# Kernel tuning notes

Hardware: AMD Instinct MI355X
Metric: run time of the kernel (lower is better)

Reference implementation:

```python
import jax, jax.numpy as jnp
from jax import lax
import numpy as np

N_GROUP = 1024   # number of FPS centroids
N_SAMPLE = 32    # neighbors per ball query
RADIUS = 0.2
BN_EPS = 1e-5    # torch BatchNorm2d default, training-mode batch stats
MLP = [64, 64, 128]
IN_CH = 6        # 3 relative xyz + 3 point features


def setup_inputs() -> dict:
    key = jax.random.key(0)
    ks = jax.random.split(key, 8)
    B, N = 16, 4096
    out = {
        "xyz": jax.random.uniform(ks[0], (B, N, 3), dtype=jnp.float32),
        "point_feature": jax.random.normal(ks[1], (B, N, 3), dtype=jnp.float32),
    }
    last = IN_CH
    for li, oc in enumerate(MLP):
        out[f"w{li}"] = jax.random.normal(ks[2 + li], (oc, last), dtype=jnp.float32) / np.float32(np.sqrt(last))
        out[f"b{li}"] = jnp.zeros((oc,), jnp.float32)
        out[f"g{li}"] = jnp.ones((oc,), jnp.float32)
        out[f"be{li}"] = jnp.zeros((oc,), jnp.float32)
        last = oc
    return out


def _fps(xyz, n_group):
    # Farthest point sampling. xyz: [B, N, 3] -> idx [B, n_group]
    B, N, _ = xyz.shape

    def step(carry, _):
        dist, farthest = carry                      # [B,N], [B]
        centroid = jnp.take_along_axis(xyz, farthest[:, None, None], axis=1)  # [B,1,3]
        d = jnp.sum((xyz - centroid) ** 2, -1)      # [B,N]
        dist = jnp.minimum(dist, d)
        nxt = jnp.argmax(dist, -1).astype(jnp.int32)
        return (dist, nxt), farthest

    init = (jnp.full((B, N), 1e10, xyz.dtype), jnp.zeros((B,), jnp.int32))
    _, idxs = lax.scan(step, init, None, length=n_group)
    return idxs.T                                    # [B, n_group]


def _ball_query(xyz, new_xyz, radius, n_sample):
    # xyz: [B,N,3], new_xyz: [B,S,3] -> idx [B,S,n_sample]
    B, N, _ = xyz.shape
    sqr = jnp.sum((new_xyz[:, :, None, :] - xyz[:, None, :, :]) ** 2, -1)  # [B,S,N]
    idx = jnp.where(sqr > radius * radius, N, jnp.arange(N, dtype=jnp.int32))
    idx = jnp.sort(idx, axis=-1)[:, :, :n_sample]    # closest-index fill like torch impl
    first = idx[:, :, :1]
    return jnp.where(idx == N, first, idx)


def reference(xyz, point_feature, w0, b0, g0, be0, w1, b1, g1, be1, w2, b2, g2, be2):
    B = xyz.shape[0]
    fps_idx = _fps(xyz, N_GROUP)                     # [B,S]
    bi = jnp.arange(B)[:, None]
    new_xyz = xyz[bi, fps_idx]                       # [B,S,3]

    idx = _ball_query(xyz, new_xyz, RADIUS, N_SAMPLE)  # [B,S,K]
    bii = jnp.arange(B)[:, None, None]
    grouped_xyz = xyz[bii, idx] - new_xyz[:, :, None, :]   # [B,S,K,3] centered
    grouped_feat = point_feature[bii, idx]                 # [B,S,K,3]
    x = jnp.concatenate([grouped_xyz, grouped_feat], -1)   # [B,S,K,6]

    # 1x1 Conv2d == per-point linear; BN over all dims but channel (training stats)
    for w, b, g, be in ((w0, b0, g0, be0), (w1, b1, g1, be1), (w2, b2, g2, be2)):
        x = jnp.einsum('bskc,oc->bsko', x, w) + b
        mu = x.mean((0, 1, 2))
        var = x.var((0, 1, 2))
        x = g * (x - mu) * lax.rsqrt(var + BN_EPS) + be
        x = jax.nn.relu(x)

    new_feature = x.max(axis=2)                      # max over n_sample -> [B,S,128]
    return new_xyz, new_feature
```

## Files before the change

kernel.cpp:

```cpp
#include <hip/hip_runtime.h>

constexpr int BATCH = 16;
constexpr int NPT   = 4096;
constexpr int NGRP  = 1024;
constexpr int NSMP  = 32;
constexpr int NPTS  = BATCH * NGRP * NSMP;
constexpr int PBLK  = 4096;
constexpr int NG    = BATCH * NGRP;

__device__ __forceinline__ float sqd(float dx, float dy, float dz) {
  return __fadd_rn(__fadd_rn(__fmul_rn(dx, dx), __fmul_rn(dy, dy)), __fmul_rn(dz, dz));
}

template <int CTRL, int RM>
__device__ __forceinline__ unsigned long long dpp_lvl(unsigned long long P) {
  const int lo = (int)(unsigned int)P;
  const int hi = (int)(unsigned int)(P >> 32);
  const int tlo = __builtin_amdgcn_update_dpp(lo, lo, CTRL, RM, 0xF, false);
  const int thi = __builtin_amdgcn_update_dpp(hi, hi, CTRL, RM, 0xF, false);
  const unsigned long long T =
      ((unsigned long long)(unsigned int)thi << 32) | (unsigned int)tlo;
  return (T > P) ? T : P;
}

__global__ __launch_bounds__(256) void fps_kernel(const float* __restrict__ xyz,
                                                  float* __restrict__ out) {
  __shared__ float sx[NPT], sy[NPT], sz[NPT];
  __shared__ float cq[NGRP * 3];
  __shared__ unsigned int ex[2][5][4];
  const int b = blockIdx.x;
  const int t = threadIdx.x;
  const float* src = xyz + (size_t)b * NPT * 3;
  for (int i = t; i < NPT; i += 256) {
    sx[i] = src[i * 3 + 0];
    sy[i] = src[i * 3 + 1];
    sz[i] = src[i * 3 + 2];
  }
  __syncthreads();
  float px[16], py[16], pz[16], dist[16];
  #pragma unroll
  for (int j = 0; j < 16; ++j) {
    const int p = j * 256 + t;
    px[j] = sx[p]; py[j] = sy[p]; pz[j] = sz[p];
    dist[j] = 1e10f;
  }
  const int w = t >> 6;
  float cx = sx[0], cy = sy[0], cz = sz[0];
  for (int step = 0; step < NGRP; ++step) {
    if (t == 0) {
      cq[step * 3 + 0] = cx;
      cq[step * 3 + 1] = cy;
      cq[step * 3 + 2] = cz;
    }
    float bestd = -1.0f; int bi = 0x7fffffff;
    #pragma unroll
    for (int j = 0; j < 16; ++j) {
      float d = sqd(px[j] - cx, py[j] - cy, pz[j] - cz);
      d = fminf(dist[j], d);
      dist[j] = d;
      if (d > bestd) { bestd = d; bi = j * 256 + t; }
    }
    const int myidx = bi;
    const unsigned long long myP =
        ((unsigned long long)__float_as_uint(bestd) << 32) |
        (unsigned long long)(unsigned int)~myidx;
    const float mx = sx[myidx], my_ = sy[myidx], mz = sz[myidx];
    unsigned long long P = myP;
    P = dpp_lvl<0xB1, 0xF>(P);
    P = dpp_lvl<0x4E, 0xF>(P);
    P = dpp_lvl<0x141, 0xF>(P);
    P = dpp_lvl<0x140, 0xF>(P);
    P = dpp_lvl<0x142, 0xA>(P);
    P = dpp_lvl<0x143, 0xC>(P);
    const unsigned int flo = (unsigned int)__builtin_amdgcn_readlane((int)(unsigned int)P, 63);
    const unsigned int fhi =
        (unsigned int)__builtin_amdgcn_readlane((int)(unsigned int)(P >> 32), 63);
    const unsigned long long PF = ((unsigned long long)fhi << 32) | flo;
    const int pb = step & 1;
    if (myP == PF) {
      ex[pb][0][w] = fhi;
      ex[pb][1][w] = flo;
      ex[pb][2][w] = __float_as_uint(mx);
      ex[pb][3][w] = __float_as_uint(my_);
      ex[pb][4][w] = __float_as_uint(mz);
    }
    __syncthreads();
    const unsigned int* e = &ex[pb][0][0];
    unsigned long long best = ((unsigned long long)e[0] << 32) | e[4];
    cx = __uint_as_float(e[8]);
    cy = __uint_as_float(e[12]);
    cz = __uint_as_float(e[16]);
    #pragma unroll
    for (int k = 1; k < 4; ++k) {
      const unsigned long long pk_ = ((unsigned long long)e[k] << 32) | e[4 + k];
      if (pk_ > best) {
        best = pk_;
        cx = __uint_as_float(e[8 + k]);
        cy = __uint_as_float(e[12 + k]);
        cz = __uint_as_float(e[16 + k]);
      }
    }
  }
  __syncthreads();
  float* outx = out + (size_t)b * NGRP * 3;
  for (int i = t; i < NGRP * 3; i += 256) outx[i] = cq[i];
}

__global__ __launch_bounds__(256) void ballq_kernel(const float* __restrict__ xyz,
                                                    const float* __restrict__ out,
                                                    int* __restrict__ idxg) {
  __shared__ float sx[NPT], sy[NPT], sz[NPT];
  const int b = blockIdx.x >> 4;
  const int sub = blockIdx.x & 15;
  const float* src = xyz + (size_t)b * NPT * 3;
  for (int i = threadIdx.x; i < NPT; i += 256) {
    sx[i] = src[i * 3 + 0];
    sy[i] = src[i * 3 + 1];
    sz[i] = src[i * 3 + 2];
  }
  __syncthreads();
  const int lane = threadIdx.x & 63;
  const int w = threadIdx.x >> 6;
  const float R2 = __fmul_rn(0.2f, 0.2f);
  for (int gi = 0; gi < 16; ++gi) {
    const int s = sub * 64 + w * 16 + gi;
    const float* c = out + ((size_t)b * NGRP + s) * 3;
    const float nx = c[0], ny = c[1], nz = c[2];
    int* og = idxg + ((size_t)b * NGRP + s) * NSMP;
    int cnt = 0, firstP = -1;
    for (int base = 0; base < NPT; base += 64) {
      const int p = base + lane;
      const float dsq = sqd(nx - sx[p], ny - sy[p], nz - sz[p]);
      const bool inr = (dsq <= R2);
      unsigned long long m = __ballot(inr);
      if (firstP < 0 && m) firstP = base + (int)__builtin_ctzll(m);
      const int rank = (int)__popcll(m & ((1ull << lane) - 1ull));
      if (inr) {
        const int pos = cnt + rank;
        if (pos < NSMP) og[pos] = p;
      }
      cnt += (int)__popcll(m);
      if (cnt >= NSMP) break;
    }
    if (cnt < NSMP) {
      for (int pos = cnt + lane; pos < NSMP; pos += 64) og[pos] = firstP;
    }
  }
}

__global__ void transpose_w3(const float* __restrict__ w3, float* __restrict__ w3t) {
  const int i = blockIdx.x * 256 + threadIdx.x;
  if (i < 128 * 64) {
    const int o = i >> 6, c = i & 63;
    w3t[c * 128 + o] = w3[i];
  }
}

__device__ __forceinline__ void gather6(const float* __restrict__ xyz, const float* __restrict__ pf,
                                        const float* __restrict__ nxyz, const int* __restrict__ idxg,
                                        int tid, float in[6]) {
  const int g = tid >> 5;
  const int b = g >> 10;
  const int i = idxg[tid];
  const float* P = xyz + ((size_t)b * NPT + i) * 3;
  const float* C = nxyz + (size_t)g * 3;
  in[0] = P[0] - C[0];
  in[1] = P[1] - C[1];
  in[2] = P[2] - C[2];
  const float* F = pf + ((size_t)b * NPT + i) * 3;
  in[3] = F[0]; in[4] = F[1]; in[5] = F[2];
}

__device__ __forceinline__ void layer1h(const float in[6], const float* __restrict__ w1,
                                        const float* __restrict__ b1, const float* __restrict__ ss1,
                                        float h1[64]) {
  #pragma unroll
  for (int o = 0; o < 64; ++o) {
    float a = b1[o];
    #pragma unroll
    for (int cc = 0; cc < 6; ++cc) a = fmaf(in[cc], w1[o * 6 + cc], a);
    h1[o] = fmaxf(0.0f, fmaf(a, ss1[o], ss1[64 + o]));
  }
}

__device__ __forceinline__ void zb_stats64(const float* zb, float* __restrict__ part,
                                           int chbase, int nch, int t, int blk) {
  const int c = t >> 1, h = t & 1;
  const float* row = zb + c * 129 + h * 64;
  float s = 0.0f, q = 0.0f;
  for (int i = 0; i < 64; ++i) {
    const float v = row[i];
    s += v;
    q = fmaf(v, v, q);
  }
  s += __shfl_xor(s, 1);
  q += __shfl_xor(q, 1);
  if (h == 0) {
    part[(size_t)(chbase + c) * PBLK + blk]       = s;
    part[(size_t)(nch + chbase + c) * PBLK + blk] = q;
  }
}

__device__ __forceinline__ void zb_stats_mm(const float* zb, float* __restrict__ part,
                                            float* __restrict__ pmax, float* __restrict__ pmin,
                                            int chbase, int nch, int t, int blk) {
  const int c = t >> 1, h = t & 1;
  const float* row = zb + c * 129 + h * 64;
  float s = 0.0f, q = 0.0f;
  float mx0 = -3.4e38f, mn0 = 3.4e38f, mx1 = -3.4e38f, mn1 = 3.4e38f;
  for (int i = 0; i < 32; ++i) {
    const float v = row[i];
    s += v; q = fmaf(v, v, q);
    mx0 = fmaxf(mx0, v); mn0 = fminf(mn0, v);
  }
  for (int i = 32; i < 64; ++i) {
    const float v = row[i];
    s += v; q = fmaf(v, v, q);
    mx1 = fmaxf(mx1, v); mn1 = fminf(mn1, v);
  }
  s += __shfl_xor(s, 1);
  q += __shfl_xor(q, 1);
  if (h == 0) {
    part[(size_t)(chbase + c) * PBLK + blk]       = s;
    part[(size_t)(nch + chbase + c) * PBLK + blk] = q;
  }
  const size_t g0 = (size_t)blk * 4 + 2 * h;
  pmax[g0 * 128 + chbase + c]       = mx0;
  pmax[(g0 + 1) * 128 + chbase + c] = mx1;
  pmin[g0 * 128 + chbase + c]       = mn0;
  pmin[(g0 + 1) * 128 + chbase + c] = mn1;
}

__global__ __launch_bounds__(256) void mom1_kernel(const float* __restrict__ xyz,
                                                   const float* __restrict__ pf,
                                                   const float* __restrict__ nxyz,
                                                   const int* __restrict__ idxg,
                                                   float* __restrict__ part) {
  const int t = threadIdx.x;
  const int base = blockIdx.x * 512 + t;
  float acc[27];
  #pragma unroll
  for (int k = 0; k < 27; ++k) acc[k] = 0.0f;
  #pragma unroll
  for (int pp = 0; pp < 2; ++pp) {
    float in[6];
    gather6(xyz, pf, nxyz, idxg, base + pp * 256, in);
    #pragma unroll
    for (int i = 0; i < 6; ++i) acc[i] += in[i];
    int k = 6;
    #pragma unroll
    for (int i = 0; i < 6; ++i)
      #pragma unroll
      for (int j = i; j < 6; ++j) { acc[k] = fmaf(in[i], in[j], acc[k]); ++k; }
  }
  #pragma unroll
  for (int off = 1; off < 64; off <<= 1) {
    #pragma unroll
    for (int k = 0; k < 27; ++k) acc[k] += __shfl_xor(acc[k], off);
  }
  const int lane = t & 63, w = t >> 6;
  if (lane == 0) {
    const int slot = blockIdx.x * 4 + w;
    #pragma unroll
    for (int k = 0; k < 27; ++k) part[k * 4096 + slot] = acc[k];
  }
}

__global__ __launch_bounds__(256) void momred_kernel(const float* __restrict__ part,
                                                     double* __restrict__ dsum) {
  const int c = blockIdx.x;
  const int t = threadIdx.x;
  double s = 0.0;
  for (int i = t; i < 4096; i += 256) s += (double)part[c * 4096 + i];
  #pragma unroll
  for (int off = 1; off < 64; off <<= 1) s += __shfl_xor(s, off);
  __shared__ double ls[4];
  const int lane = t & 63, w = t >> 6;
  if (lane == 0) ls[w] = s;
  __syncthreads();
  if (t == 0) dsum[c] = ls[0] + ls[1] + ls[2] + ls[3];
}

__global__ __launch_bounds__(64) void finalize1_kernel(const double* __restrict__ dsum,
                                                       const float* __restrict__ w1,
                                                       const float* __restrict__ b1,
                                                       const float* __restrict__ g,
                                                       const float* __restrict__ be,
                                                       float* __restrict__ ss) {
  __shared__ double sm[27];
  const int t = threadIdx.x;
  if (t < 27) sm[t] = dsum[t];
  __syncthreads();
  const double N = (double)NPTS;
  double wv[6];
  #pragma unroll
  for (int i = 0; i < 6; ++i) wv[i] = (double)w1[t * 6 + i];
  double mean_wx = 0.0;
  #pragma unroll
  for (int i = 0; i < 6; ++i) mean_wx += wv[i] * sm[i];
  mean_wx /= N;
  const double bb = (double)b1[t];
  const double mu = mean_wx + bb;
  double qq = 0.0;
  int k = 6;
  #pragma unroll
  for (int i = 0; i < 6; ++i)
    #pragma unroll
    for (int j = i; j < 6; ++j) {
      qq += (i == j ? 1.0 : 2.0) * wv[i] * wv[j] * (sm[k] / N);
      ++k;
    }
  const double Ez2 = qq + 2.0 * bb * mean_wx + bb * bb;
  const double var = Ez2 - mu * mu;
  const double inv = 1.0 / sqrt(var + 1e-5);
  ss[t]      = (float)((double)g[t] * inv);
  ss[64 + t] = (float)((double)be[t] - (double)g[t] * mu * inv);
}

__global__ __launch_bounds__(256) void reduce_kernel(const float* __restrict__ part, int nblk, int nch,
                                                     const float* __restrict__ g, const float* __restrict__ be,
                                                     float* __restrict__ ss) {
  const int c = blockIdx.x;
  const int t = threadIdx.x;
  double s = 0.0, q = 0.0;
  for (int i = t; i < nblk; i += 256) {
    s += (double)part[(size_t)c * nblk + i];
    q += (double)part[(size_t)(nch + c) * nblk + i];
  }
  #pragma unroll
  for (int off = 1; off < 64; off <<= 1) {
    s += __shfl_xor(s, off);
    q += __shfl_xor(q, off);
  }
  __shared__ double ls[4], lq[4];
  const int lane = t & 63, w = t >> 6;
  if (lane == 0) { ls[w] = s; lq[w] = q; }
  __syncthreads();
  if (t == 0) {
    const double S = ls[0] + ls[1] + ls[2] + ls[3];
    const double Q = lq[0] + lq[1] + lq[2] + lq[3];
    const double n = (double)NPTS;
    const double mu = S / n;
    const double var = Q / n - mu * mu;
    const double inv = 1.0 / sqrt(var + 1e-5);
    ss[c]       = (float)((double)g[c] * inv);
    ss[nch + c] = (float)((double)be[c] - (double)g[c] * mu * inv);
  }
}

__global__ __launch_bounds__(128) void pass2_kernel(const float* __restrict__ xyz, const float* __restrict__ pf,
                                                    const float* __restrict__ nxyz, const int* __restrict__ idxg,
                                                    const float* __restrict__ w1, const float* __restrict__ b1,
                                                    const float* __restrict__ ss1,
                                                    const float* __restrict__ w2, const float* __restrict__ b2,
                                                    float* __restrict__ part) {
  __shared__ float zb[64 * 129];
  const int t = threadIdx.x;
  const int tid = blockIdx.x * 128 + t;
  float in[6];
  gather6(xyz, pf, nxyz, idxg, tid, in);
  float h1[64];
  layer1h(in, w1, b1, ss1, h1);
  for (int o = 0; o < 64; ++o) {
    float a = b2[o];
    #pragma unroll
    for (int cc = 0; cc < 64; ++cc) a = fmaf(h1[cc], w2[o * 64 + cc], a);
    zb[o * 129 + t] = a;
  }
  __syncthreads();
  zb_stats64(zb, part, 0, 64, t, blockIdx.x);
}

__device__ __forceinline__ void compute_z3(const float* __restrict__ xyz, const float* __restrict__ pf,
                                           const float* __restrict__ nxyz, const int* __restrict__ idxg,
                                           const float* __restrict__ w1, const float* __restrict__ b1,
                                           const float* __restrict__ ss1,
                                           const float* __restrict__ w2, const float* __restrict__ b2,
                                           const float* __restrict__ ss2,
                                           const float* __restrict__ w3t, const float* __restrict__ b3,
                                           float* shm, int t, int tid, float acc[128]) {
  float in[6];
  gather6(xyz, pf, nxyz, idxg, tid, in);
  float h1[64];
  layer1h(in, w1, b1, ss1, h1);
  float* hrow = shm + t * 65;
  for (int o = 0; o < 64; ++o) {
    float a = b2[o];
    #pragma unroll
    for (int cc = 0; cc < 64; ++cc) a = fmaf(h1[cc], w2[o * 64 + cc], a);
    hrow[o] = fmaxf(0.0f, fmaf(a, ss2[o], ss2[64 + o]));
  }
  #pragma unroll
  for (int o = 0; o < 128; ++o) acc[o] = b3[o];
  for (int cc = 0; cc < 64; ++cc) {
    const float hc = hrow[cc];
    const float* wrow = w3t + cc * 128;
    #pragma unroll
    for (int o = 0; o < 128; ++o) acc[o] = fmaf(hc, wrow[o], acc[o]);
  }
}

__global__ __launch_bounds__(128) void pass3_kernel(const float* __restrict__ xyz, const float* __restrict__ pf,
                                                    const float* __restrict__ nxyz, const int* __restrict__ idxg,
                                                    const float* __restrict__ w1, const float* __restrict__ b1,
                                                    const float* __restrict__ ss1,
                                                    const float* __restrict__ w2, const float* __restrict__ b2,
                                                    const float* __restrict__ ss2,
                                                    const float* __restrict__ w3t, const float* __restrict__ b3,
                                                    float* __restrict__ part,
                                                    float* __restrict__ pmax, float* __restrict__ pmin) {
  __shared__ float shm[8320];
  const int t = threadIdx.x;
  const int tid = blockIdx.x * 128 + t;
  float acc[128];
  compute_z3(xyz, pf, nxyz, idxg, w1, b1, ss1, w2, b2, ss2, w3t, b3, shm, t, tid, acc);
  __syncthreads();
  #pragma unroll
  for (int o = 0; o < 64; ++o) shm[o * 129 + t] = acc[o];
  __syncthreads();
  if (pmax) zb_stats_mm(shm, part, pmax, pmin, 0, 128, t, blockIdx.x);
  else      zb_stats64(shm, part, 0, 128, t, blockIdx.x);
  __syncthreads();
  #pragma unroll
  for (int o = 0; o < 64; ++o) shm[o * 129 + t] = acc[64 + o];
  __syncthreads();
  if (pmax) zb_stats_mm(shm, part, pmax, pmin, 64, 128, t, blockIdx.x);
  else      zb_stats64(shm, part, 64, 128, t, blockIdx.x);
}

__global__ __launch_bounds__(256) void pass4f_kernel(const float* __restrict__ pmax,
                                                     const float* __restrict__ pmin,
                                                     const float* __restrict__ ss3,
                                                     float* __restrict__ outF) {
  const int i = blockIdx.x * 256 + threadIdx.x;
  const int c = i & 127;
  const float a = ss3[c], bb = ss3[128 + c];
  const float z = (a >= 0.0f) ? pmax[i] : pmin[i];
  outF[i] = fmaxf(0.0f, fmaf(z, a, bb));
}

__global__ __launch_bounds__(128) void pass4_kernel(const float* __restrict__ xyz, const float* __restrict__ pf,
                                                    const float* __restrict__ nxyz, const int* __restrict__ idxg,
                                                    const float* __restrict__ w1, const float* __restrict__ b1,
                                                    const float* __restrict__ ss1,
                                                    const float* __restrict__ w2, const float* __restrict__ b2,
                                                    const float* __restrict__ ss2,
                                                    const float* __restrict__ w3t, const float* __restrict__ b3,
                                                    const float* __restrict__ ss3,
                                                    float* __restrict__ outF) {
  __shared__ float shm[8320];
  const int t = threadIdx.x;
  const int tid = blockIdx.x * 128 + t;
  float acc[128];
  compute_z3(xyz, pf, nxyz, idxg, w1, b1, ss1, w2, b2, ss2, w3t, b3, shm, t, tid, acc);
  #pragma unroll
  for (int o = 0; o < 128; ++o)
    acc[o] = fmaxf(0.0f, fmaf(acc[o], ss3[o], ss3[128 + o]));
  __syncthreads();
  const int c4 = t & 63, gp = t >> 6;
  #pragma unroll
  for (int o = 0; o < 64; ++o) shm[o * 129 + t] = acc[o];
  __syncthreads();
  #pragma unroll
  for (int gs = 0; gs < 2; ++gs) {
    const int g = gp * 2 + gs;
    const float* row = shm + c4 * 129 + g * 32;
    float m = row[0];
    for (int i = 1; i < 32; ++i) m = fmaxf(m, row[i]);
    outF[((size_t)blockIdx.x * 4 + g) * 128 + c4] = m;
  }
  __syncthreads();
  #pragma unroll
  for (int o = 0; o < 64; ++o) shm[o * 129 + t] = acc[64 + o];
  __syncthreads();
  #pragma unroll
  for (int gs = 0; gs < 2; ++gs) {
    const int g = gp * 2 + gs;
    const float* row = shm + c4 * 129 + g * 32;
    float m = row[0];
    for (int i = 1; i < 32; ++i) m = fmaxf(m, row[i]);
    outF[((size_t)blockIdx.x * 4 + g) * 128 + 64 + c4] = m;
  }
}

extern "C" void kernel_launch(void* const* d_in, const int* in_sizes, int n_in,
                              void* d_out, int out_size, void* d_ws, size_t ws_size,
                              hipStream_t stream) {
  (void)in_sizes; (void)n_in; (void)out_size;
  const float* xyz = (const float*)d_in[0];
  const float* pf  = (const float*)d_in[1];
  const float* w1  = (const float*)d_in[2];
  const float* b1  = (const float*)d_in[3];
  const float* g1  = (const float*)d_in[4];
  const float* be1 = (const float*)d_in[5];
  const float* w2  = (const float*)d_in[6];
  const float* b2  = (const float*)d_in[7];
  const float* g2  = (const float*)d_in[8];
  const float* be2 = (const float*)d_in[9];
  const float* w3  = (const float*)d_in[10];
  const float* b3  = (const float*)d_in[11];
  const float* g3  = (const float*)d_in[12];
  const float* be3 = (const float*)d_in[13];
  float* out = (float*)d_out;

  int*    idxg = (int*)d_ws;
  float*  p1   = (float*)((char*)d_ws + (size_t)NPTS * 4);
  float*  ss1  = p1 + (size_t)PBLK * 128;
  float*  p2   = ss1 + 128;
  float*  ss2  = p2 + (size_t)PBLK * 128;
  float*  p3   = ss2 + 128;
  float*  ss3  = p3 + (size_t)PBLK * 256;
  float*  w3t  = ss3 + 256;
  double* dsum = (double*)(w3t + 8192);
  float*  pmax = (float*)(dsum + 32);
  float*  pmin = pmax + (size_t)NG * 128;
  const size_t needed = (size_t)((char*)(pmin + (size_t)NG * 128) - (char*)d_ws);
  const bool fast4 = (ws_size >= needed);

  transpose_w3<<<32, 256, 0, stream>>>(w3, w3t);
  fps_kernel<<<BATCH, 256, 0, stream>>>(xyz, out);
  ballq_kernel<<<BATCH * 16, 256, 0, stream>>>(xyz, out, idxg);
  mom1_kernel<<<1024, 256, 0, stream>>>(xyz, pf, out, idxg, p1);
  momred_kernel<<<27, 256, 0, stream>>>(p1, dsum);
  finalize1_kernel<<<1, 64, 0, stream>>>(dsum, w1, b1, g1, be1, ss1);
  pass2_kernel<<<PBLK, 128, 0, stream>>>(xyz, pf, out, idxg, w1, b1, ss1, w2, b2, p2);
  reduce_kernel<<<64, 256, 0, stream>>>(p2, PBLK, 64, g2, be2, ss2);
  pass3_kernel<<<PBLK, 128, 0, stream>>>(xyz, pf, out, idxg, w1, b1, ss1, w2, b2, ss2, w3t, b3, p3,
                                         fast4 ? pmax : nullptr, fast4 ? pmin : nullptr);
  reduce_kernel<<<128, 256, 0, stream>>>(p3, PBLK, 128, g3, be3, ss3);
  float* outF = out + (size_t)BATCH * NGRP * 3;
  if (fast4) {
    pass4f_kernel<<<(NG * 128) / 256, 256, 0, stream>>>(pmax, pmin, ss3, outF);
  } else {
    pass4_kernel<<<PBLK, 128, 0, stream>>>(xyz, pf, out, idxg, w1, b1, ss1, w2, b2, ss2, w3t, b3, ss3,
                                           outF);
  }
}
```

Measured before the change: 1.383 ms.

## Fuse layer-1 moment stats into ball query and cache layer-2 preactivations in bf16

Computes the first-layer input moment sums inside the ball-query kernel from shared-memory coordinates, which removes the separate mom1 kernel and its global gather. Pass2 now also stores the layer-2 pre-activations as bf16 in workspace, and pass3 reads them back instead of recomputing the gather plus layers 1-2. That trades a 64x64 matmul per point for a bandwidth-bound bf16 read and write, and lowers the precision of the stored intermediate, which can shift results slightly.

```diff
diff --git a/kernel.cpp b/kernel.cpp
--- a/kernel.cpp
+++ b/kernel.cpp
@@ -1,4 +1,5 @@
 #include <hip/hip_runtime.h>
+#include <hip/hip_bf16.h>
 
 constexpr int BATCH = 16;
 constexpr int NPT   = 4096;
@@ -107,9 +108,13 @@
 }
 
 __global__ __launch_bounds__(256) void ballq_kernel(const float* __restrict__ xyz,
+                                                    const float* __restrict__ pf,
                                                     const float* __restrict__ out,
-                                                    int* __restrict__ idxg) {
+                                                    int* __restrict__ idxg,
+                                                    float* __restrict__ part) {
   __shared__ float sx[NPT], sy[NPT], sz[NPT];
+  __shared__ int   sel[64 * NSMP];
+  __shared__ float cent[64][3];
   const int b = blockIdx.x >> 4;
   const int sub = blockIdx.x & 15;
   const float* src = xyz + (size_t)b * NPT * 3;
@@ -123,10 +128,13 @@
   const int w = threadIdx.x >> 6;
   const float R2 = __fmul_rn(0.2f, 0.2f);
   for (int gi = 0; gi < 16; ++gi) {
-    const int s = sub * 64 + w * 16 + gi;
+    const int g = w * 16 + gi;
+    const int s = sub * 64 + g;
     const float* c = out + ((size_t)b * NGRP + s) * 3;
     const float nx = c[0], ny = c[1], nz = c[2];
+    if (lane == 0) { cent[g][0] = nx; cent[g][1] = ny; cent[g][2] = nz; }
     int* og = idxg + ((size_t)b * NGRP + s) * NSMP;
+    int* sg = sel + g * NSMP;
     int cnt = 0, firstP = -1;
     for (int base = 0; base < NPT; base += 64) {
       const int p = base + lane;
@@ -137,14 +145,50 @@
       const int rank = (int)__popcll(m & ((1ull << lane) - 1ull));
       if (inr) {
         const int pos = cnt + rank;
-        if (pos < NSMP) og[pos] = p;
+        if (pos < NSMP) { og[pos] = p; sg[pos] = p; }
       }
       cnt += (int)__popcll(m);
       if (cnt >= NSMP) break;
     }
     if (cnt < NSMP) {
-      for (int pos = cnt + lane; pos < NSMP; pos += 64) og[pos] = firstP;
-    }
+      for (int pos = cnt + lane; pos < NSMP; pos += 64) { og[pos] = firstP; sg[pos] = firstP; }
+    }
+  }
+  __syncthreads();
+  float acc[27];
+  #pragma unroll
+  for (int k = 0; k < 27; ++k) acc[k] = 0.0f;
+  const float* pfb = pf + (size_t)b * NPT * 3;
+  const int g2 = threadIdx.x >> 2;
+  const float c0 = cent[g2][0], c1 = cent[g2][1], c2 = cent[g2][2];
+  #pragma unroll
+  for (int ii = 0; ii < 8; ++ii) {
+    const int si = threadIdx.x * 8 + ii;
+    const int i = sel[si];
+    float in[6];
+    in[0] = sx[i] - c0;
+    in[1] = sy[i] - c1;
+    in[2] = sz[i] - c2;
+    in[3] = pfb[i * 3 + 0];
+    in[4] = pfb[i * 3 + 1];
+    in[5] = pfb[i * 3 + 2];
+    #pragma unroll
+    for (int k = 0; k < 6; ++k) acc[k] += in[k];
+    int k = 6;
+    #pragma unroll
+    for (int a = 0; a < 6; ++a)
+      #pragma unroll
+      for (int bb = a; bb < 6; ++bb) { acc[k] = fmaf(in[a], in[bb], acc[k]); ++k; }
+  }
+  #pragma unroll
+  for (int off = 1; off < 64; off <<= 1) {
+    #pragma unroll
+    for (int k = 0; k < 27; ++k) acc[k] += __shfl_xor(acc[k], off);
+  }
+  if (lane == 0) {
+    const int slot = blockIdx.x * 4 + w;
+    #pragma unroll
+    for (int k = 0; k < 27; ++k) part[k * 1024 + slot] = acc[k];
   }
 }
 
@@ -231,47 +275,12 @@
   pmin[(g0 + 1) * 128 + chbase + c] = mn1;
 }
 
-__global__ __launch_bounds__(256) void mom1_kernel(const float* __restrict__ xyz,
-                                                   const float* __restrict__ pf,
-                                                   const float* __restrict__ nxyz,
-                                                   const int* __restrict__ idxg,
-                                                   float* __restrict__ part) {
-  const int t = threadIdx.x;
-  const int base = blockIdx.x * 512 + t;
-  float acc[27];
-  #pragma unroll
-  for (int k = 0; k < 27; ++k) acc[k] = 0.0f;
-  #pragma unroll
-  for (int pp = 0; pp < 2; ++pp) {
-    float in[6];
-    gather6(xyz, pf, nxyz, idxg, base + pp * 256, in);
-    #pragma unroll
-    for (int i = 0; i < 6; ++i) acc[i] += in[i];
-    int k = 6;
-    #pragma unroll
-    for (int i = 0; i < 6; ++i)
-      #pragma unroll
-      for (int j = i; j < 6; ++j) { acc[k] = fmaf(in[i], in[j], acc[k]); ++k; }
-  }
-  #pragma unroll
-  for (int off = 1; off < 64; off <<= 1) {
-    #pragma unroll
-    for (int k = 0; k < 27; ++k) acc[k] += __shfl_xor(acc[k], off);
-  }
-  const int lane = t & 63, w = t >> 6;
-  if (lane == 0) {
-    const int slot = blockIdx.x * 4 + w;
-    #pragma unroll
-    for (int k = 0; k < 27; ++k) part[k * 4096 + slot] = acc[k];
-  }
-}
-
 __global__ __launch_bounds__(256) void momred_kernel(const float* __restrict__ part,
-                                                     double* __restrict__ dsum) {
+                                                     double* __restrict__ dsum, int n) {
   const int c = blockIdx.x;
   const int t = threadIdx.x;
   double s = 0.0;
-  for (int i = t; i < 4096; i += 256) s += (double)part[c * 4096 + i];
+  for (int i = t; i < n; i += 256) s += (double)part[c * n + i];
   #pragma unroll
   for (int off = 1; off < 64; off <<= 1) s += __shfl_xor(s, off);
   __shared__ double ls[4];
@@ -353,7 +362,8 @@
                                                     const float* __restrict__ w1, const float* __restrict__ b1,
                                                     const float* __restrict__ ss1,
                                                     const float* __restrict__ w2, const float* __restrict__ b2,
-                                                    float* __restrict__ part) {
+                                                    float* __restrict__ part,
+                                                    __hip_bfloat16* __restrict__ z2c) {
   __shared__ float zb[64 * 129];
   const int t = threadIdx.x;
   const int tid = blockIdx.x * 128 + t;
@@ -366,6 +376,7 @@
     #pragma unroll
     for (int cc = 0; cc < 64; ++cc) a = fmaf(h1[cc], w2[o * 64 + cc], a);
     zb[o * 129 + t] = a;
+    if (z2c) z2c[(size_t)o * NPTS + tid] = __float2bfloat16(a);
   }
   __syncthreads();
   zb_stats64(zb, part, 0, 64, t, blockIdx.x);
@@ -378,17 +389,26 @@
                                            const float* __restrict__ w2, const float* __restrict__ b2,
                                            const float* __restrict__ ss2,
                                            const float* __restrict__ w3t, const float* __restrict__ b3,
+                                           const __hip_bfloat16* __restrict__ z2c,
                                            float* shm, int t, int tid, float acc[128]) {
-  float in[6];
-  gather6(xyz, pf, nxyz, idxg, tid, in);
-  float h1[64];
-  layer1h(in, w1, b1, ss1, h1);
   float* hrow = shm + t * 65;
-  for (int o = 0; o < 64; ++o) {
-    float a = b2[o];
-    #pragma unroll
-    for (int cc = 0; cc < 64; ++cc) a = fmaf(h1[cc], w2[o * 64 + cc], a);
-    hrow[o] = fmaxf(0.0f, fmaf(a, ss2[o], ss2[64 + o]));
+  if (z2c) {
+    #pragma unroll
+    for (int o = 0; o < 64; ++o) {
+      const float z = __bfloat162float(z2c[(size_t)o * NPTS + tid]);
+      hrow[o] = fmaxf(0.0f, fmaf(z, ss2[o], ss2[64 + o]));
+    }
+  } else {
+    float in[6];
+    gather6(xyz, pf, nxyz, idxg, tid, in);
+    float h1[64];
+    layer1h(in, w1, b1, ss1, h1);
+    for (int o = 0; o < 64; ++o) {
+      float a = b2[o];
+      #pragma unroll
+      for (int cc = 0; cc < 64; ++cc) a = fmaf(h1[cc], w2[o * 64 + cc], a);
+      hrow[o] = fmaxf(0.0f, fmaf(a, ss2[o], ss2[64 + o]));
+    }
   }
   #pragma unroll
   for (int o = 0; o < 128; ++o) acc[o] = b3[o];
@@ -407,13 +427,14 @@
                                                     const float* __restrict__ w2, const float* __restrict__ b2,
                                                     const float* __restrict__ ss2,
                                                     const float* __restrict__ w3t, const float* __restrict__ b3,
+                                                    const __hip_bfloat16* __restrict__ z2c,
                                                     float* __restrict__ part,
                                                     float* __restrict__ pmax, float* __restrict__ pmin) {
   __shared__ float shm[8320];
   const int t = threadIdx.x;
   const int tid = blockIdx.x * 128 + t;
   float acc[128];
-  compute_z3(xyz, pf, nxyz, idxg, w1, b1, ss1, w2, b2, ss2, w3t, b3, shm, t, tid, acc);
+  compute_z3(xyz, pf, nxyz, idxg, w1, b1, ss1, w2, b2, ss2, w3t, b3, z2c, shm, t, tid, acc);
   __syncthreads();
   #pragma unroll
   for (int o = 0; o < 64; ++o) shm[o * 129 + t] = acc[o];
@@ -446,13 +467,14 @@
                                                     const float* __restrict__ w2, const float* __restrict__ b2,
                                                     const float* __restrict__ ss2,
                                                     const float* __restrict__ w3t, const float* __restrict__ b3,
+                                                    const __hip_bfloat16* __restrict__ z2c,
                                                     const float* __restrict__ ss3,
                                                     float* __restrict__ outF) {
   __shared__ float shm[8320];
   const int t = threadIdx.x;
   const int tid = blockIdx.x * 128 + t;
   float acc[128];
-  compute_z3(xyz, pf, nxyz, idxg, w1, b1, ss1, w2, b2, ss2, w3t, b3, shm, t, tid, acc);
+  compute_z3(xyz, pf, nxyz, idxg, w1, b1, ss1, w2, b2, ss2, w3t, b3, z2c, shm, t, tid, acc);
   #pragma unroll
   for (int o = 0; o < 128; ++o)
     acc[o] = fmaxf(0.0f, fmaf(acc[o], ss3[o], ss3[128 + o]));
@@ -514,25 +536,28 @@
   double* dsum = (double*)(w3t + 8192);
   float*  pmax = (float*)(dsum + 32);
   float*  pmin = pmax + (size_t)NG * 128;
-  const size_t needed = (size_t)((char*)(pmin + (size_t)NG * 128) - (char*)d_ws);
-  const bool fast4 = (ws_size >= needed);
+  __hip_bfloat16* z2c = (__hip_bfloat16*)(pmin + (size_t)NG * 128);
+  const size_t needed4 = (size_t)((char*)z2c - (char*)d_ws);
+  const size_t needed3 = needed4 + (size_t)NPTS * 64 * sizeof(__hip_bfloat16);
+  const bool fast4 = (ws_size >= needed4);
+  const bool fast3 = (ws_size >= needed3);
+  __hip_bfloat16* z2cp = fast3 ? z2c : nullptr;
 
   transpose_w3<<<32, 256, 0, stream>>>(w3, w3t);
   fps_kernel<<<BATCH, 256, 0, stream>>>(xyz, out);
-  ballq_kernel<<<BATCH * 16, 256, 0, stream>>>(xyz, out, idxg);
-  mom1_kernel<<<1024, 256, 0, stream>>>(xyz, pf, out, idxg, p1);
-  momred_kernel<<<27, 256, 0, stream>>>(p1, dsum);
+  ballq_kernel<<<BATCH * 16, 256, 0, stream>>>(xyz, pf, out, idxg, p1);
+  momred_kernel<<<27, 256, 0, stream>>>(p1, dsum, 1024);
   finalize1_kernel<<<1, 64, 0, stream>>>(dsum, w1, b1, g1, be1, ss1);
-  pass2_kernel<<<PBLK, 128, 0, stream>>>(xyz, pf, out, idxg, w1, b1, ss1, w2, b2, p2);
+  pass2_kernel<<<PBLK, 128, 0, stream>>>(xyz, pf, out, idxg, w1, b1, ss1, w2, b2, p2, z2cp);
   reduce_kernel<<<64, 256, 0, stream>>>(p2, PBLK, 64, g2, be2, ss2);
-  pass3_kernel<<<PBLK, 128, 0, stream>>>(xyz, pf, out, idxg, w1, b1, ss1, w2, b2, ss2, w3t, b3, p3,
-                                         fast4 ? pmax : nullptr, fast4 ? pmin : nullptr);
+  pass3_kernel<<<PBLK, 128, 0, stream>>>(xyz, pf, out, idxg, w1, b1, ss1, w2, b2, ss2, w3t, b3, z2cp,
+                                         p3, fast4 ? pmax : nullptr, fast4 ? pmin : nullptr);
   reduce_kernel<<<128, 256, 0, stream>>>(p3, PBLK, 128, g3, be3, ss3);
   float* outF = out + (size_t)BATCH * NGRP * 3;
   if (fast4) {
     pass4f_kernel<<<(NG * 128) / 256, 256, 0, stream>>>(pmax, pmin, ss3, outF);
   } else {
-    pass4_kernel<<<PBLK, 128, 0, stream>>>(xyz, pf, out, idxg, w1, b1, ss1, w2, b2, ss2, w3t, b3, ss3,
-                                           outF);
-  }
-}
+    pass4_kernel<<<PBLK, 128, 0, stream>>>(xyz, pf, out, idxg, w1, b1, ss1, w2, b2, ss2, w3t, b3,
+                                           z2cp, ss3, outF);
+  }
+}
```

New measurement: 1.187 ms. 1.17x faster.
